# Kernel tuning notes

Measured on AMD Instinct MI355X. Metric: run time of the kernel, lower is better.

Reference implementation:

```python
import jax, jax.numpy as jnp
import numpy as np

B, K, H, W = 16, 64, 160, 160
EPS = 1e-5


def setup_inputs() -> dict:
    key = jax.random.key(0)
    k1, k2 = jax.random.split(key)
    # keypoints[..., 0] = x in [0, W-1], keypoints[..., 1] = y in [0, H-1]
    kp = jax.random.uniform(k1, (B, K, 2), dtype=jnp.float32)
    keypoints = kp * jnp.array([W - 1.0, H - 1.0], dtype=jnp.float32)
    DetectionMap = jax.random.uniform(k2, (B, K, H, W), dtype=jnp.float32)
    return {
        "keypoints": keypoints,
        "reconDetectionMap_std_x": jnp.float32(6.0),
        "reconDetectionMap_std_y": jnp.float32(6.0),
        "correlation": jnp.float32(0.1),
        "DetectionMap": DetectionMap,
    }


def reference(keypoints, reconDetectionMap_std_x, reconDetectionMap_std_y, correlation, DetectionMap):
    sx = reconDetectionMap_std_x
    sy = reconDetectionMap_std_y
    rho = correlation
    Bv, Kv, Hv, Wv = DetectionMap.shape

    one_m_rho2 = 1.0 - rho * rho
    den = 1.0 / (2.0 * jnp.pi * sx * sy * jnp.sqrt(one_m_rho2))
    num1 = -1.0 / (2.0 * one_m_rho2)

    ii = jnp.arange(Hv, dtype=keypoints.dtype)  # rows (y)
    jj = jnp.arange(Wv, dtype=keypoints.dtype)  # cols (x)
    # dy: [B,K,H,1], dx: [B,K,1,W] -> broadcast to [B,K,H,W] only inside num2
    dy = ii[None, None, :, None] - keypoints[:, :, 1][:, :, None, None]
    dx = jj[None, None, None, :] - keypoints[:, :, 0][:, :, None, None]

    num2 = (dy * dy) / (sy * sy) + (dx * dx) / (sx * sx) \
        - (2.0 * rho / (sx * sy)) * dy * dx  # [B,K,H,W]
    scoreMap = den * jnp.exp(num1 * num2)  # [B,K,H,W]

    denom = jnp.sum(scoreMap, axis=1, keepdims=True) + EPS  # [B,1,H,W]
    return scoreMap / denom
```

## Files before the change

### kernel.cpp

```cpp
#include <hip/hip_runtime.h>

#define KK 64
#define HH 160
#define WW 160
#define HWPIX (HH * WW)
#define EPSF 1e-5f

__global__ __launch_bounds__(256) void recon_confmap_kernel(
    const float* __restrict__ kp,
    const float* __restrict__ sx_p,
    const float* __restrict__ sy_p,
    const float* __restrict__ rho_p,
    float* __restrict__ out)
{
    __shared__ float2 skp[KK];

    const int b   = blockIdx.y;
    const int tid = threadIdx.x;

    if (tid < KK) {
        skp[tid] = ((const float2*)(kp + (size_t)b * KK * 2))[tid];
    }

    const float sx  = sx_p[0];
    const float sy  = sy_p[0];
    const float rho = rho_p[0];
    __syncthreads();

    const float L2E   = 1.44269504088896340736f;
    const float omr2  = 1.0f - rho * rho;
    const float num1  = -0.5f / omr2;
    const float ca    = num1 / (sy * sy) * L2E;
    const float cb    = num1 / (sx * sx) * L2E;
    const float cc    = num1 * (-2.0f * rho / (sx * sy)) * L2E;
    const float epsod = EPSF * (2.0f * 3.14159265358979323846f * sx * sy * sqrtf(omr2));

    const int p  = blockIdx.x * 256 + tid;
    const int i  = p / WW;
    const int j  = p - i * WW;
    const float fi = (float)i;
    const float fj = (float)j;

    float s[KK];
    float sum = 0.0f;
#pragma unroll
    for (int k = 0; k < KK; ++k) {
        const float dy  = fi - skp[k].y;
        const float dx  = fj - skp[k].x;
        const float arg = fmaf(ca * dy, dy, fmaf(cb * dx, dx, cc * dy * dx));
        const float e   = __builtin_amdgcn_exp2f(arg);
        s[k] = e;
        sum += e;
    }

    const float inv = 1.0f / (sum + epsod);

    float* op = out + (size_t)b * KK * HWPIX + p;
#pragma unroll
    for (int k = 0; k < KK; ++k) {
        op[(size_t)k * HWPIX] = s[k] * inv;
    }
}

extern "C" void kernel_launch(void* const* d_in, const int* in_sizes, int n_in,
                              void* d_out, int out_size, void* d_ws, size_t ws_size,
                              hipStream_t stream) {
    const float* kp    = (const float*)d_in[0];
    const float* sx_p  = (const float*)d_in[1];
    const float* sy_p  = (const float*)d_in[2];
    const float* rho_p = (const float*)d_in[3];
    float* out = (float*)d_out;

    const int B = in_sizes[0] / (KK * 2);
    dim3 grid(HWPIX / 256, B);
    recon_confmap_kernel<<<grid, 256, 0, stream>>>(kp, sx_p, sy_p, rho_p, out);
}
```

Before: 168.2 us.

## Split into denominator pass and vectorized per-keypoint score pass

Splits the fused kernel in two. The first kernel computes the per-pixel inverse denominator into workspace, with two pixels per thread. The second kernel recomputes each Gaussian per (batch, keypoint, pixel) and writes float4 stores, replacing the 64-register array and the scalar strided stores of the old kernel. This targets output store efficiency and register pressure. The cost is recomputing every exp, one extra kernel launch, and a workspace round trip.

```diff
diff --git a/kernel.cpp b/kernel.cpp
--- a/kernel.cpp
+++ b/kernel.cpp
@@ -1,4 +1,5 @@
 #include <hip/hip_runtime.h>
+#include <math.h>
 
 #define KK 64
 #define HH 160
@@ -6,60 +7,115 @@
 #define HWPIX (HH * WW)
 #define EPSF 1e-5f
 
-__global__ __launch_bounds__(256) void recon_confmap_kernel(
+__global__ __launch_bounds__(256) void denom_kernel(
     const float* __restrict__ kp,
     const float* __restrict__ sx_p,
     const float* __restrict__ sy_p,
     const float* __restrict__ rho_p,
-    float* __restrict__ out)
+    float* __restrict__ invden)
 {
     __shared__ float2 skp[KK];
 
     const int b   = blockIdx.y;
     const int tid = threadIdx.x;
-
-    if (tid < KK) {
-        skp[tid] = ((const float2*)(kp + (size_t)b * KK * 2))[tid];
-    }
+    if (tid < KK) skp[tid] = ((const float2*)(kp + (size_t)b * KK * 2))[tid];
 
     const float sx  = sx_p[0];
     const float sy  = sy_p[0];
     const float rho = rho_p[0];
     __syncthreads();
 
-    const float L2E   = 1.44269504088896340736f;
-    const float omr2  = 1.0f - rho * rho;
-    const float num1  = -0.5f / omr2;
-    const float ca    = num1 / (sy * sy) * L2E;
-    const float cb    = num1 / (sx * sx) * L2E;
-    const float cc    = num1 * (-2.0f * rho / (sx * sy)) * L2E;
+    const float L2E  = 1.44269504088896340736f;
+    const float omr2 = 1.0f - rho * rho;
+    const float num1 = -0.5f / omr2;
+    const float ca   = num1 / (sy * sy) * L2E;
+    const float cb   = num1 / (sx * sx) * L2E;
+    const float cc   = num1 * (-2.0f * rho / (sx * sy)) * L2E;
     const float epsod = EPSF * (2.0f * 3.14159265358979323846f * sx * sy * sqrtf(omr2));
 
-    const int p  = blockIdx.x * 256 + tid;
-    const int i  = p / WW;
-    const int j  = p - i * WW;
-    const float fi = (float)i;
-    const float fj = (float)j;
+    const int p0 = blockIdx.x * 512 + tid * 2;
+    const int i  = p0 / WW;
+    const int j  = p0 - i * WW;
+    const float fi  = (float)i;
+    const float fj0 = (float)j;
+    const float fj1 = fj0 + 1.0f;
 
-    float s[KK];
-    float sum = 0.0f;
+    float sum0 = 0.0f, sum1 = 0.0f;
 #pragma unroll
     for (int k = 0; k < KK; ++k) {
-        const float dy  = fi - skp[k].y;
-        const float dx  = fj - skp[k].x;
-        const float arg = fmaf(ca * dy, dy, fmaf(cb * dx, dx, cc * dy * dx));
-        const float e   = __builtin_amdgcn_exp2f(arg);
-        s[k] = e;
-        sum += e;
+        const float dy   = fi - skp[k].y;
+        const float ady  = ca * dy * dy;
+        const float cdy  = cc * dy;
+        const float dx0  = fj0 - skp[k].x;
+        const float dx1  = fj1 - skp[k].x;
+        const float a0   = fmaf(cdy, dx0, fmaf(cb * dx0, dx0, ady));
+        const float a1   = fmaf(cdy, dx1, fmaf(cb * dx1, dx1, ady));
+        sum0 += __builtin_amdgcn_exp2f(a0);
+        sum1 += __builtin_amdgcn_exp2f(a1);
     }
 
-    const float inv = 1.0f / (sum + epsod);
+    float2 r;
+    r.x = 1.0f / (sum0 + epsod);
+    r.y = 1.0f / (sum1 + epsod);
+    *(float2*)(invden + (size_t)b * HWPIX + p0) = r;
+}
 
-    float* op = out + (size_t)b * KK * HWPIX + p;
-#pragma unroll
-    for (int k = 0; k < KK; ++k) {
-        op[(size_t)k * HWPIX] = s[k] * inv;
+__global__ __launch_bounds__(256) void score_kernel(
+    const float* __restrict__ kp,
+    const float* __restrict__ sx_p,
+    const float* __restrict__ sy_p,
+    const float* __restrict__ rho_p,
+    const float* __restrict__ invden,
+    float* __restrict__ out)
+{
+    const int b = blockIdx.z;
+    const int k = blockIdx.y;
+
+    const float2 kpk = ((const float2*)(kp + (size_t)b * KK * 2))[k];
+    const float sx  = sx_p[0];
+    const float sy  = sy_p[0];
+    const float rho = rho_p[0];
+
+    const float L2E  = 1.44269504088896340736f;
+    const float omr2 = 1.0f - rho * rho;
+    const float num1 = -0.5f / omr2;
+    const float ca   = num1 / (sy * sy) * L2E;
+    const float cb   = num1 / (sx * sx) * L2E;
+    const float cc   = num1 * (-2.0f * rho / (sx * sy)) * L2E;
+
+    const int p0 = blockIdx.x * 1024 + threadIdx.x * 4;
+    const int i  = p0 / WW;
+    const int j  = p0 - i * WW;
+
+    const float dy  = (float)i - kpk.y;
+    const float ady = ca * dy * dy;
+    const float cdy = cc * dy;
+    const float dx0 = (float)j - kpk.x;
+
+    const float4 inv = *(const float4*)(invden + (size_t)b * HWPIX + p0);
+
+    float4 o;
+    {
+        const float a = fmaf(cdy, dx0, fmaf(cb * dx0, dx0, ady));
+        o.x = __builtin_amdgcn_exp2f(a) * inv.x;
     }
+    {
+        const float dx = dx0 + 1.0f;
+        const float a = fmaf(cdy, dx, fmaf(cb * dx, dx, ady));
+        o.y = __builtin_amdgcn_exp2f(a) * inv.y;
+    }
+    {
+        const float dx = dx0 + 2.0f;
+        const float a = fmaf(cdy, dx, fmaf(cb * dx, dx, ady));
+        o.z = __builtin_amdgcn_exp2f(a) * inv.z;
+    }
+    {
+        const float dx = dx0 + 3.0f;
+        const float a = fmaf(cdy, dx, fmaf(cb * dx, dx, ady));
+        o.w = __builtin_amdgcn_exp2f(a) * inv.w;
+    }
+
+    *(float4*)(out + ((size_t)(b * KK + k) * HWPIX) + p0) = o;
 }
 
 extern "C" void kernel_launch(void* const* d_in, const int* in_sizes, int n_in,
@@ -69,9 +125,14 @@
     const float* sx_p  = (const float*)d_in[1];
     const float* sy_p  = (const float*)d_in[2];
     const float* rho_p = (const float*)d_in[3];
-    float* out = (float*)d_out;
+    float* out    = (float*)d_out;
+    float* invden = (float*)d_ws;
 
     const int B = in_sizes[0] / (KK * 2);
-    dim3 grid(HWPIX / 256, B);
-    recon_confmap_kernel<<<grid, 256, 0, stream>>>(kp, sx_p, sy_p, rho_p, out);
+
+    dim3 grid1(HWPIX / 512, B);
+    denom_kernel<<<grid1, 256, 0, stream>>>(kp, sx_p, sy_p, rho_p, invden);
+
+    dim3 grid2(HWPIX / 1024, KK, B);
+    score_kernel<<<grid2, 256, 0, stream>>>(kp, sx_p, sy_p, rho_p, invden, out);
 }
```

Measured after the change: 177.2 us. +5.4%, slower.

## Process four pixels per thread, recompute exponentials, use vector nontemporal stores

Applied to the files above, without the earlier changes.

Each thread now handles four adjacent pixels in a row, sharing the per-keypoint dy terms across them. It stops holding 64 exponentials in registers and recomputes them in a second pass after the normalising sums are known. The output is written as 16-byte nontemporal vector stores. The aim is to cut register pressure, widen the memory transactions on this write-bound kernel and bypass the cache for streaming output, at the cost of doubling the exp work. Because 160 is divisible by 4, each group of four pixels stays within one row.

```diff
diff --git a/kernel.cpp b/kernel.cpp
--- a/kernel.cpp
+++ b/kernel.cpp
@@ -6,7 +6,9 @@
 #define HWPIX (HH * WW)
 #define EPSF 1e-5f
 
-__global__ __launch_bounds__(256) void recon_confmap_kernel(
+typedef float vfloat4 __attribute__((ext_vector_type(4)));
+
+__global__ __launch_bounds__(256) void recon_confmap_fused(
     const float* __restrict__ kp,
     const float* __restrict__ sx_p,
     const float* __restrict__ sy_p,
@@ -17,48 +19,64 @@
 
     const int b   = blockIdx.y;
     const int tid = threadIdx.x;
-
-    if (tid < KK) {
-        skp[tid] = ((const float2*)(kp + (size_t)b * KK * 2))[tid];
-    }
+    if (tid < KK) skp[tid] = ((const float2*)(kp + (size_t)b * KK * 2))[tid];
 
     const float sx  = sx_p[0];
     const float sy  = sy_p[0];
     const float rho = rho_p[0];
     __syncthreads();
 
-    const float L2E   = 1.44269504088896340736f;
-    const float omr2  = 1.0f - rho * rho;
-    const float num1  = -0.5f / omr2;
-    const float ca    = num1 / (sy * sy) * L2E;
-    const float cb    = num1 / (sx * sx) * L2E;
-    const float cc    = num1 * (-2.0f * rho / (sx * sy)) * L2E;
+    const float L2E  = 1.44269504088896340736f;
+    const float omr2 = 1.0f - rho * rho;
+    const float num1 = -0.5f / omr2;
+    const float ca   = num1 / (sy * sy) * L2E;
+    const float cb   = num1 / (sx * sx) * L2E;
+    const float cc   = num1 * (-2.0f * rho / (sx * sy)) * L2E;
     const float epsod = EPSF * (2.0f * 3.14159265358979323846f * sx * sy * sqrtf(omr2));
 
-    const int p  = blockIdx.x * 256 + tid;
-    const int i  = p / WW;
-    const int j  = p - i * WW;
-    const float fi = (float)i;
-    const float fj = (float)j;
+    const int p0 = blockIdx.x * 1024 + tid * 4;
+    const int i  = p0 / WW;
+    const int j  = p0 - i * WW;
+    const float fi  = (float)i;
+    const float fj  = (float)j;
 
-    float s[KK];
-    float sum = 0.0f;
+    float s0 = 0.0f, s1 = 0.0f, s2 = 0.0f, s3 = 0.0f;
 #pragma unroll
     for (int k = 0; k < KK; ++k) {
         const float dy  = fi - skp[k].y;
-        const float dx  = fj - skp[k].x;
-        const float arg = fmaf(ca * dy, dy, fmaf(cb * dx, dx, cc * dy * dx));
-        const float e   = __builtin_amdgcn_exp2f(arg);
-        s[k] = e;
-        sum += e;
+        const float ady = ca * dy * dy;
+        const float cdy = cc * dy;
+        const float dx0 = fj - skp[k].x;
+        const float dx1 = dx0 + 1.0f;
+        const float dx2 = dx0 + 2.0f;
+        const float dx3 = dx0 + 3.0f;
+        s0 += __builtin_amdgcn_exp2f(fmaf(cdy, dx0, fmaf(cb * dx0, dx0, ady)));
+        s1 += __builtin_amdgcn_exp2f(fmaf(cdy, dx1, fmaf(cb * dx1, dx1, ady)));
+        s2 += __builtin_amdgcn_exp2f(fmaf(cdy, dx2, fmaf(cb * dx2, dx2, ady)));
+        s3 += __builtin_amdgcn_exp2f(fmaf(cdy, dx3, fmaf(cb * dx3, dx3, ady)));
     }
 
-    const float inv = 1.0f / (sum + epsod);
+    const float i0 = 1.0f / (s0 + epsod);
+    const float i1 = 1.0f / (s1 + epsod);
+    const float i2 = 1.0f / (s2 + epsod);
+    const float i3 = 1.0f / (s3 + epsod);
 
-    float* op = out + (size_t)b * KK * HWPIX + p;
+    float* op = out + (size_t)b * KK * HWPIX + p0;
 #pragma unroll
     for (int k = 0; k < KK; ++k) {
-        op[(size_t)k * HWPIX] = s[k] * inv;
+        const float dy  = fi - skp[k].y;
+        const float ady = ca * dy * dy;
+        const float cdy = cc * dy;
+        const float dx0 = fj - skp[k].x;
+        const float dx1 = dx0 + 1.0f;
+        const float dx2 = dx0 + 2.0f;
+        const float dx3 = dx0 + 3.0f;
+        vfloat4 o;
+        o.x = __builtin_amdgcn_exp2f(fmaf(cdy, dx0, fmaf(cb * dx0, dx0, ady))) * i0;
+        o.y = __builtin_amdgcn_exp2f(fmaf(cdy, dx1, fmaf(cb * dx1, dx1, ady))) * i1;
+        o.z = __builtin_amdgcn_exp2f(fmaf(cdy, dx2, fmaf(cb * dx2, dx2, ady))) * i2;
+        o.w = __builtin_amdgcn_exp2f(fmaf(cdy, dx3, fmaf(cb * dx3, dx3, ady))) * i3;
+        __builtin_nontemporal_store(o, (vfloat4*)(op + (size_t)k * HWPIX));
     }
 }
 
@@ -72,6 +90,6 @@
     float* out = (float*)d_out;
 
     const int B = in_sizes[0] / (KK * 2);
-    dim3 grid(HWPIX / 256, B);
-    recon_confmap_kernel<<<grid, 256, 0, stream>>>(kp, sx_p, sy_p, rho_p, out);
+    dim3 grid(HWPIX / 1024, B);
+    recon_confmap_fused<<<grid, 256, 0, stream>>>(kp, sx_p, sy_p, rho_p, out);
 }
```

Result: slower. 174.3 us (+3.6%).
